# Performance work log

Measured on AMD Instinct MI355X. Metric: run time of the kernel, lower is better.

Reference implementation:

```python
import jax, jax.numpy as jnp
import numpy as np

L, B, D, Di, N, H, P, K, M, V = 4, 8, 2048, 4096, 128, 64, 64, 4, 8, 50288
Cch = Di + 2 * N           # conv channels = 4352
Dout = 2 * Di + 2 * N + H  # in_proj out = 8512
EPS = 1e-5


def _rms(x, w):
    return x * jax.lax.rsqrt(jnp.mean(x * x, axis=-1, keepdims=True) + EPS) * w


def setup_inputs() -> dict:
    key = jax.random.key(0)
    ks = jax.random.split(key, 16)
    s = 0.02
    return {
        "input_ids": jax.random.randint(ks[0], (B, 1), 0, V),
        "emb": jax.random.normal(ks[1], (V, D)) * s,
        "in_proj_w": jax.random.normal(ks[2], (L, D, Dout)) * s,
        "conv_w": jax.random.normal(ks[3], (L, Cch, K)) * s,
        "conv_b": jax.random.normal(ks[4], (L, Cch)) * s,
        "A_log": jax.random.normal(ks[5], (L, H)) * 0.5,
        "dt_bias": jax.random.normal(ks[6], (L, H)) * 0.5,
        "D_param": jax.random.normal(ks[7], (L, H)) * 0.5,
        "mixer_norm_w": jnp.ones((L, Di)),
        "out_proj_w": jax.random.normal(ks[8], (L, Di, D)) * s,
        "layer_norm_w": jnp.ones((L, D)),
        "norm_f_w": jnp.ones((D,)),
        "W_mc": jax.random.normal(ks[9], (L, M + 1)).at[:, -1].set(5.0),
        "conv_state": jax.random.normal(ks[10], (L, B, Cch, K)) * 0.1,
        "ssm_state": jax.random.normal(ks[11], (L, B, H, P, N)) * 0.1,
        "cached_states": jax.random.normal(ks[12], (L, B, M, H, P, N)) * 0.1,
    }


def reference(input_ids, emb, in_proj_w, conv_w, conv_b, A_log, dt_bias, D_param,
              mixer_norm_w, out_proj_w, layer_norm_w, norm_f_w, W_mc,
              conv_state, ssm_state, cached_states):
    ids = input_ids[:, 0]              # (B,)
    res = emb[ids]                     # (B, D) token embedding gather
    for l in range(L):
        xn = _rms(res, layer_norm_w[l])
        zxbcdt = xn @ in_proj_w[l]     # (B, Dout)
        z = zxbcdt[:, :Di]
        xBC = zxbcdt[:, Di:Di + Cch]
        dt = zxbcdt[:, Di + Cch:]
        # circular conv-state shift + depthwise conv over kernel dim
        cs = jnp.concatenate([conv_state[l][:, :, 1:], xBC[:, :, None]], axis=-1)
        xBC = jax.nn.silu(jnp.sum(cs * conv_w[l][None], axis=-1) + conv_b[l])
        x, Bm, Cm = xBC[:, :Di], xBC[:, Di:Di + N], xBC[:, Di + N:]
        dt = jax.nn.softplus(dt + dt_bias[l])                 # (B, H)
        dA = jnp.exp(dt * (-jnp.exp(A_log[l])))               # (B, H)
        x = x.reshape(B, H, P)
        dBx = jnp.einsum('bh,bn,bhp->bhpn', dt, Bm, x)        # (B,H,P,N)
        ssm = ssm_state[l] * dA[:, :, None, None] + dBx       # (B,H,P,N)
        # softmax-weighted fusion of cached segment states + current state
        w = jax.nn.softmax(W_mc[l])                           # (M+1,)
        fused = jnp.einsum('bmhpn,m->bhpn', cached_states[l], w[:-1]) + w[-1] * ssm
        y = jnp.einsum('bhpn,bn->bhp', fused, Cm) + D_param[l][None, :, None] * x
        y = y.reshape(B, Di)
        y = _rms(y * jax.nn.silu(z), mixer_norm_w[l])         # gated RMSNorm
        res = res + y @ out_proj_w[l]
    res = _rms(res, norm_f_w)
    logits = res @ emb.T               # tied lm_head
    return logits[:, None, :]          # (B, 1, V)
```

## Files before the change

kernel.cpp:

```cpp
#include <hip/hip_runtime.h>
#include <hip/hip_bf16.h>
#include <math.h>

#define LN 4
#define B_ 8
#define D_ 2048
#define DI 4096
#define N_ 128
#define H_ 64
#define P_ 64
#define K_ 4
#define M_ 8
#define V_ 50288
#define CCH (DI + 2*N_)
#define DOUT (2*DI + 2*N_ + H_)
#define EPSF 1e-5f
#define KT_IN 32
#define KT_OUT 128

typedef float f32x4 __attribute__((ext_vector_type(4)));

__device__ inline float wave_sum(float v) {
  #pragma unroll
  for (int off = 32; off > 0; off >>= 1) v += __shfl_xor(v, off, 64);
  return v;
}

__device__ inline float fold_reduce8(const float a[8], int lane) {
  float t0[4];
  #pragma unroll
  for (int r = 0; r < 4; ++r) {
    float keep = (lane & 1) ? a[2*r+1] : a[2*r];
    float send = (lane & 1) ? a[2*r]   : a[2*r+1];
    t0[r] = keep + __shfl_xor(send, 1, 64);
  }
  float t1[2];
  #pragma unroll
  for (int r = 0; r < 2; ++r) {
    float keep = (lane & 2) ? t0[2*r+1] : t0[2*r];
    float send = (lane & 2) ? t0[2*r]   : t0[2*r+1];
    t1[r] = keep + __shfl_xor(send, 2, 64);
  }
  float keep = (lane & 4) ? t1[1] : t1[0];
  float send = (lane & 4) ? t1[0] : t1[1];
  float u = keep + __shfl_xor(send, 4, 64);
  u += __shfl_xor(u, 8, 64);
  u += __shfl_xor(u, 16, 64);
  u += __shfl_xor(u, 32, 64);
  return u;
}

__global__ __launch_bounds__(256)
void k_rmsnorm(const float* __restrict__ in, const float* __restrict__ w,
               float* __restrict__ out, const int* __restrict__ ids,
               const float* __restrict__ emb, float* __restrict__ res_out) {
  __shared__ float lds[4];
  int b = blockIdx.x, tid = threadIdx.x;
  const float* row = ids ? (emb + (size_t)ids[b] * D_) : (in + (size_t)b * D_);
  f32x4 v0 = *reinterpret_cast<const f32x4*>(row + tid * 8);
  f32x4 v1 = *reinterpret_cast<const f32x4*>(row + tid * 8 + 4);
  if (res_out) {
    *reinterpret_cast<f32x4*>(res_out + (size_t)b * D_ + tid * 8)     = v0;
    *reinterpret_cast<f32x4*>(res_out + (size_t)b * D_ + tid * 8 + 4) = v1;
  }
  float ss = v0[0]*v0[0] + v0[1]*v0[1] + v0[2]*v0[2] + v0[3]*v0[3]
           + v1[0]*v1[0] + v1[1]*v1[1] + v1[2]*v1[2] + v1[3]*v1[3];
  float wsum = wave_sum(ss);
  int lane = tid & 63, wid = tid >> 6;
  if (lane == 0) lds[wid] = wsum;
  __syncthreads();
  float tot = lds[0] + lds[1] + lds[2] + lds[3];
  float scale = rsqrtf(tot / (float)D_ + EPSF);
  f32x4 w0 = *reinterpret_cast<const f32x4*>(w + tid * 8);
  f32x4 w1 = *reinterpret_cast<const f32x4*>(w + tid * 8 + 4);
  f32x4 o0 = v0 * scale * w0, o1 = v1 * scale * w1;
  *reinterpret_cast<f32x4*>(out + (size_t)b * D_ + tid * 8)     = o0;
  *reinterpret_cast<f32x4*>(out + (size_t)b * D_ + tid * 8 + 4) = o1;
}

__global__ void k_inproj1(const float* __restrict__ xn, const float* __restrict__ W,
                          float* __restrict__ pin) {
  __shared__ float xs[8][64];
  int jt = blockIdx.x % 9, kt = blockIdx.x / 9;
  int k0 = kt * 64;
  for (int i = threadIdx.x; i < 8 * 64; i += 256) {
    int r = i >> 6, kk = i & 63;
    xs[r][kk] = xn[r * D_ + k0 + kk];
  }
  __syncthreads();
  int j = jt * 1024 + threadIdx.x * 4;
  if (j >= DOUT) return;
  f32x4 acc[8];
  #pragma unroll
  for (int r = 0; r < 8; ++r) acc[r] = (f32x4)0.f;
  const float* Wp = W + (size_t)k0 * DOUT + j;
  for (int kk = 0; kk < 64; ++kk) {
    f32x4 w4 = __builtin_nontemporal_load(
        reinterpret_cast<const f32x4*>(Wp + (size_t)kk * DOUT));
    #pragma unroll
    for (int r = 0; r < 8; ++r) acc[r] += w4 * xs[r][kk];
  }
  #pragma unroll
  for (int r = 0; r < 8; ++r)
    *reinterpret_cast<f32x4*>(&pin[((size_t)kt * 8 + r) * DOUT + j]) = acc[r];
}

__global__ __launch_bounds__(256)
void k_inproj2_conv(const float* __restrict__ pin, const float* __restrict__ conv_state,
                    const float* __restrict__ conv_w, const float* __restrict__ conv_b,
                    const float* __restrict__ A_log, const float* __restrict__ dt_bias,
                    const float* __restrict__ W_mc,
                    float* __restrict__ zx, float* __restrict__ xbc,
                    float* __restrict__ dts, float* __restrict__ dav,
                    float* __restrict__ wmc) {
  const int TOT4 = B_ * DOUT / 4;
  int t = blockIdx.x * 256 + threadIdx.x;
  if (t >= TOT4) return;
  f32x4 s = (f32x4)0.f;
  const f32x4* p4 = reinterpret_cast<const f32x4*>(pin) + t;
  #pragma unroll 8
  for (int kt = 0; kt < KT_IN; ++kt) s += p4[(size_t)kt * TOT4];
  reinterpret_cast<f32x4*>(zx)[t] = s;
  int c4 = t * 4;
  int b = c4 / DOUT;
  int c = c4 - b * DOUT;
  #pragma unroll
  for (int e = 0; e < 4; ++e) {
    int ce = c + e;
    if (ce >= DI && ce < DI + CCH) {
      int cc = ce - DI;
      f32x4 cs4 = *reinterpret_cast<const f32x4*>(conv_state + ((size_t)b * CCH + cc) * K_);
      f32x4 cw4 = *reinterpret_cast<const f32x4*>(conv_w + (size_t)cc * K_);
      float v = cs4[1] * cw4[0] + cs4[2] * cw4[1] + cs4[3] * cw4[2]
              + s[e] * cw4[3] + conv_b[cc];
      xbc[b * CCH + cc] = v / (1.f + expf(-v));
    } else if (ce >= DI + CCH) {
      int h = ce - DI - CCH;
      float x = s[e] + dt_bias[h];
      float sp = (x > 20.f) ? x : log1pf(expf(x));
      dts[b * 64 + h] = sp;
      dav[b * 64 + h] = expf(-expf(A_log[h]) * sp);
    }
  }
  if (t == 0) {
    float mx = -1e30f;
    for (int i = 0; i < M_ + 1; ++i) mx = fmaxf(mx, W_mc[i]);
    float e2[M_ + 1], sum = 0.f;
    for (int i = 0; i < M_ + 1; ++i) { e2[i] = expf(W_mc[i] - mx); sum += e2[i]; }
    for (int i = 0; i < M_ + 1; ++i) wmc[i] = e2[i] / sum;
  }
}

__global__ __launch_bounds__(256)
void k_state(const float* __restrict__ xbc, const float* __restrict__ dts,
             const float* __restrict__ dav, const float* __restrict__ Dp_,
             const float* __restrict__ wmc, const float* __restrict__ ssm,
             const float* __restrict__ cached, float* __restrict__ y) {
  int wg = blockIdx.x * 4 + (threadIdx.x >> 6);
  int lane = threadIdx.x & 63;
  int b = wg >> 11;
  int h = (wg >> 5) & 63;
  int pp = wg & 31;
  int hf = lane >> 5, il = lane & 31;
  int p = pp * 2 + hf;
  float xv  = xbc[b * CCH + h * 64 + p];
  float dtv = dts[b * 64 + h];
  float da  = dav[b * 64 + h];
  float w8  = wmc[8];
  const f32x4* xb4 = reinterpret_cast<const f32x4*>(xbc);
  f32x4 B4 = xb4[b * (CCH / 4) + DI / 4 + il];
  f32x4 C4 = xb4[b * (CCH / 4) + DI / 4 + N_ / 4 + il];
  const f32x4* sp4 = reinterpret_cast<const f32x4*>(ssm) +
                     ((size_t)((b * H_ + h) * P_ + p)) * (N_ / 4) + il;
  const f32x4* cp4 = reinterpret_cast<const f32x4*>(cached) +
                     ((size_t)(((b * M_) * H_ + h) * P_ + p)) * (N_ / 4) + il;
  f32x4 s4 = __builtin_nontemporal_load(sp4);
  f32x4 f4 = (s4 * da + B4 * (dtv * xv)) * w8;
  #pragma unroll
  for (int m = 0; m < 8; ++m) {
    f32x4 c4 = __builtin_nontemporal_load(cp4 + (size_t)m * (H_ * P_ * N_ / 4));
    f4 += c4 * wmc[m];
  }
  f4 *= C4;
  float acc = f4[0] + f4[1] + f4[2] + f4[3];
  #pragma unroll
  for (int off = 1; off < 32; off <<= 1) acc += __shfl_xor(acc, off, 64);
  if (il == 0) y[b * DI + h * 64 + p] = acc + Dp_[h] * xv;
}

__global__ void k_gatednorm(const float* __restrict__ y, const float* __restrict__ zx,
                            const float* __restrict__ mnw, float* __restrict__ yg) {
  __shared__ float lds[8];
  int b = blockIdx.x;
  float tv[16];
  float ss = 0.f;
  #pragma unroll
  for (int t = 0; t < 16; ++t) {
    int i = threadIdx.x + t * 256;
    float z = zx[b * DOUT + i];
    float v = y[b * DI + i] * (z / (1.f + expf(-z)));
    tv[t] = v; ss += v * v;
  }
  float wsum = wave_sum(ss);
  int lane = threadIdx.x & 63, wid = threadIdx.x >> 6;
  if (lane == 0) lds[wid] = wsum;
  __syncthreads();
  float tot = lds[0] + lds[1] + lds[2] + lds[3];
  float scale = rsqrtf(tot / (float)DI + EPSF);
  #pragma unroll
  for (int t = 0; t < 16; ++t) {
    int i = threadIdx.x + t * 256;
    yg[b * DI + i] = tv[t] * scale * mnw[i];
  }
}

__global__ void k_outproj1(const float* __restrict__ yg, const float* __restrict__ W,
                           float* __restrict__ pout) {
  __shared__ float xs[8][32];
  int jt = blockIdx.x & 1, kt = blockIdx.x >> 1;
  int k0 = kt * 32;
  for (int i = threadIdx.x; i < 8 * 32; i += 256) {
    int r = i >> 5, kk = i & 31;
    xs[r][kk] = yg[r * DI + k0 + kk];
  }
  __syncthreads();
  int j = jt * 1024 + threadIdx.x * 4;
  f32x4 acc[8];
  #pragma unroll
  for (int r = 0; r < 8; ++r) acc[r] = (f32x4)0.f;
  const float* Wp = W + (size_t)k0 * D_ + j;
  for (int kk = 0; kk < 32; ++kk) {
    f32x4 w4 = __builtin_nontemporal_load(
        reinterpret_cast<const f32x4*>(Wp + (size_t)kk * D_));
    #pragma unroll
    for (int r = 0; r < 8; ++r) acc[r] += w4 * xs[r][kk];
  }
  #pragma unroll
  for (int r = 0; r < 8; ++r)
    *reinterpret_cast<f32x4*>(&pout[((size_t)kt * 8 + r) * D_ + j]) = acc[r];
}

__global__ __launch_bounds__(256)
void k_outproj2(const float* __restrict__ pout, float* __restrict__ res,
                float* __restrict__ zbuf, int zn4) {
  if (zbuf) {
    f32x4* z4 = reinterpret_cast<f32x4*>(zbuf);
    for (int i = blockIdx.x * 256 + threadIdx.x; i < zn4; i += 16 * 256)
      z4[i] = (f32x4)0.f;
  }
  const int TOT4 = B_ * D_ / 4;
  int t = blockIdx.x * 256 + threadIdx.x;
  f32x4 s = (f32x4)0.f;
  const f32x4* p4 = reinterpret_cast<const f32x4*>(pout) + t;
  #pragma unroll 8
  for (int kt = 0; kt < KT_OUT; ++kt) s += p4[(size_t)kt * TOT4];
  reinterpret_cast<f32x4*>(res)[t] += s;
}

#define SL_ 4
#define KS_ (D_ / SL_)
#define NVB16 (V_ / 16)
__global__ __launch_bounds__(256)
void k_logits(const float* __restrict__ xn, const float* __restrict__ emb,
              float* __restrict__ out) {
  __shared__ f32x4 xs[8][KS_ / 4];
  int s = blockIdx.x & 3, vb = blockIdx.x >> 2;
  const f32x4* xn4 = reinterpret_cast<const f32x4*>(xn);
  for (int i = threadIdx.x; i < 8 * (KS_ / 4); i += 256) {
    int r = i >> 7, q = i & 127;
    xs[r][q] = xn4[r * (D_ / 4) + s * (KS_ / 4) + q];
  }
  __syncthreads();
  int wid = threadIdx.x >> 6, lane = threadIdx.x & 63;
  int v0 = vb * 16 + wid * 4;
  const f32x4* e4 = reinterpret_cast<const f32x4*>(emb);
  #pragma unroll
  for (int vv = 0; vv < 4; ++vv) {
    int v = v0 + vv;
    const f32x4* ep = e4 + (size_t)v * (D_ / 4) + s * (KS_ / 4);
    float acc[8] = {0,0,0,0,0,0,0,0};
    #pragma unroll
    for (int st = 0; st < KS_ / 256; ++st) {
      int c = st * 64 + lane;
      f32x4 e = __builtin_nontemporal_load(ep + c);
      #pragma unroll
      for (int r = 0; r < 8; ++r) {
        f32x4 x = xs[r][c];
        acc[r] += e[0]*x[0] + e[1]*x[1] + e[2]*x[2] + e[3]*x[3];
      }
    }
    float u = fold_reduce8(acc, lane);
    if (lane < 8) atomicAdd(&out[(size_t)lane * V_ + v], u);
  }
}

extern "C" void kernel_launch(void* const* d_in, const int* in_sizes, int n_in,
                              void* d_out, int out_size, void* d_ws, size_t ws_size,
                              hipStream_t stream) {
  const int*   ids    = (const int*)  d_in[0];
  const float* emb    = (const float*)d_in[1];
  const float* inW    = (const float*)d_in[2];
  const float* convW  = (const float*)d_in[3];
  const float* convB  = (const float*)d_in[4];
  const float* Alog   = (const float*)d_in[5];
  const float* dtB    = (const float*)d_in[6];
  const float* Dpar   = (const float*)d_in[7];
  const float* mnw    = (const float*)d_in[8];
  const float* outW   = (const float*)d_in[9];
  const float* lnw    = (const float*)d_in[10];
  const float* nfw    = (const float*)d_in[11];
  const float* Wmc    = (const float*)d_in[12];
  const float* convS  = (const float*)d_in[13];
  const float* ssmS   = (const float*)d_in[14];
  const float* cached = (const float*)d_in[15];
  float* out = (float*)d_out;
  float* ws  = (float*)d_ws;

  float* res  = ws;
  float* xn   = ws + 16384;
  float* zx   = ws + 32768;
  float* xbc  = ws + 100864;
  float* dts  = ws + 135680;
  float* dav  = ws + 136192;
  float* wmc  = ws + 136704;
  float* y    = ws + 136768;
  float* yg   = ws + 169536;
  float* pin  = ws + 202304;
  float* pout = ws + 2381376;

  for (int l = 0; l < LN; ++l) {
    if (l == 0)
      k_rmsnorm<<<8, 256, 0, stream>>>(nullptr, lnw, xn, ids, emb, res);
    else
      k_rmsnorm<<<8, 256, 0, stream>>>(res, lnw + (size_t)l * D_, xn,
                                       nullptr, nullptr, nullptr);
    k_inproj1<<<288, 256, 0, stream>>>(xn, inW + (size_t)l * D_ * DOUT, pin);
    k_inproj2_conv<<<67, 256, 0, stream>>>(pin,
        convS + (size_t)l * B_ * CCH * K_, convW + (size_t)l * CCH * K_,
        convB + (size_t)l * CCH, Alog + l * H_, dtB + l * H_, Wmc + l * (M_ + 1),
        zx, xbc, dts, dav, wmc);
    k_state<<<4096, 256, 0, stream>>>(xbc, dts, dav, Dpar + l * H_, wmc,
        ssmS + (size_t)l * B_ * H_ * P_ * N_,
        cached + (size_t)l * B_ * M_ * H_ * P_ * N_, y);
    k_gatednorm<<<8, 256, 0, stream>>>(y, zx, mnw + (size_t)l * DI, yg);
    k_outproj1<<<256, 256, 0, stream>>>(yg, outW + (size_t)l * DI * D_, pout);
    k_outproj2<<<16, 256, 0, stream>>>(pout, res,
                                       (l == LN - 1) ? out : nullptr,
                                       B_ * V_ / 4);
  }
  k_rmsnorm<<<8, 256, 0, stream>>>(res, nfw, xn, nullptr, nullptr, nullptr);
  k_logits<<<NVB16 * SL_, 256, 0, stream>>>(xn, emb, out);
}
```

Measured before the change: 477.7 us.

## Fuse RMSNorm into in-proj, widen out-proj reduction, replace logit atomics with two-pass sum

The per-layer RMSNorm launch is removed. Each in-proj block now recomputes the row norms for all 8 rows and normalises its own 64-column slice. The out-proj reduction grows from 16 to 64 blocks with an in-block split-K tree, and the embedding gather for layer 0 is folded into the residual update. Logit atomics plus the output zero-fill are replaced by partial-sum stores and a separate reduction kernel. This trades fewer launches and no atomics for redundant full-row norm reads in all 288 in-proj blocks and extra partial logit traffic.

```diff
diff --git a/kernel.cpp b/kernel.cpp
--- a/kernel.cpp
+++ b/kernel.cpp
@@ -52,17 +52,12 @@
 
 __global__ __launch_bounds__(256)
 void k_rmsnorm(const float* __restrict__ in, const float* __restrict__ w,
-               float* __restrict__ out, const int* __restrict__ ids,
-               const float* __restrict__ emb, float* __restrict__ res_out) {
+               float* __restrict__ out) {
   __shared__ float lds[4];
   int b = blockIdx.x, tid = threadIdx.x;
-  const float* row = ids ? (emb + (size_t)ids[b] * D_) : (in + (size_t)b * D_);
+  const float* row = in + (size_t)b * D_;
   f32x4 v0 = *reinterpret_cast<const f32x4*>(row + tid * 8);
   f32x4 v1 = *reinterpret_cast<const f32x4*>(row + tid * 8 + 4);
-  if (res_out) {
-    *reinterpret_cast<f32x4*>(res_out + (size_t)b * D_ + tid * 8)     = v0;
-    *reinterpret_cast<f32x4*>(res_out + (size_t)b * D_ + tid * 8 + 4) = v1;
-  }
   float ss = v0[0]*v0[0] + v0[1]*v0[1] + v0[2]*v0[2] + v0[3]*v0[3]
            + v1[0]*v1[0] + v1[1]*v1[1] + v1[2]*v1[2] + v1[3]*v1[3];
   float wsum = wave_sum(ss);
@@ -78,17 +73,39 @@
   *reinterpret_cast<f32x4*>(out + (size_t)b * D_ + tid * 8 + 4) = o1;
 }
 
-__global__ void k_inproj1(const float* __restrict__ xn, const float* __restrict__ W,
-                          float* __restrict__ pin) {
+__global__ __launch_bounds__(256)
+void k_inproj1(const float* __restrict__ res, const int* __restrict__ ids,
+               const float* __restrict__ emb, const float* __restrict__ lnw,
+               const float* __restrict__ W, float* __restrict__ pin) {
   __shared__ float xs[8][64];
+  __shared__ float sred[4][8];
+  int tid = threadIdx.x, lane = tid & 63, wid = tid >> 6;
   int jt = blockIdx.x % 9, kt = blockIdx.x / 9;
   int k0 = kt * 64;
-  for (int i = threadIdx.x; i < 8 * 64; i += 256) {
+  float ssq[8];
+  #pragma unroll
+  for (int r = 0; r < 8; ++r) {
+    const float* row = ids ? (emb + (size_t)ids[r] * D_) : (res + (size_t)r * D_);
+    f32x4 a = *reinterpret_cast<const f32x4*>(row + tid * 8);
+    f32x4 c = *reinterpret_cast<const f32x4*>(row + tid * 8 + 4);
+    ssq[r] = a[0]*a[0] + a[1]*a[1] + a[2]*a[2] + a[3]*a[3]
+           + c[0]*c[0] + c[1]*c[1] + c[2]*c[2] + c[3]*c[3];
+  }
+  #pragma unroll
+  for (int r = 0; r < 8; ++r) {
+    float wsum = wave_sum(ssq[r]);
+    if (lane == 0) sred[wid][r] = wsum;
+  }
+  __syncthreads();
+  for (int i = tid; i < 8 * 64; i += 256) {
     int r = i >> 6, kk = i & 63;
-    xs[r][kk] = xn[r * D_ + k0 + kk];
-  }
-  __syncthreads();
-  int j = jt * 1024 + threadIdx.x * 4;
+    const float* row = ids ? (emb + (size_t)ids[r] * D_) : (res + (size_t)r * D_);
+    float tot = sred[0][r] + sred[1][r] + sred[2][r] + sred[3][r];
+    float scale = rsqrtf(tot / (float)D_ + EPSF);
+    xs[r][kk] = row[k0 + kk] * scale * lnw[k0 + kk];
+  }
+  __syncthreads();
+  int j = jt * 1024 + tid * 4;
   if (j >= DOUT) return;
   f32x4 acc[8];
   #pragma unroll
@@ -242,19 +259,30 @@
 
 __global__ __launch_bounds__(256)
 void k_outproj2(const float* __restrict__ pout, float* __restrict__ res,
-                float* __restrict__ zbuf, int zn4) {
-  if (zbuf) {
-    f32x4* z4 = reinterpret_cast<f32x4*>(zbuf);
-    for (int i = blockIdx.x * 256 + threadIdx.x; i < zn4; i += 16 * 256)
-      z4[i] = (f32x4)0.f;
-  }
+                const int* __restrict__ ids, const float* __restrict__ emb) {
+  __shared__ f32x4 red[256];
   const int TOT4 = B_ * D_ / 4;
-  int t = blockIdx.x * 256 + threadIdx.x;
+  int tid = threadIdx.x;
+  int pos = blockIdx.x * 64 + (tid & 63);
+  int kq = tid >> 6;
+  const f32x4* p4 = reinterpret_cast<const f32x4*>(pout) + pos;
   f32x4 s = (f32x4)0.f;
-  const f32x4* p4 = reinterpret_cast<const f32x4*>(pout) + t;
   #pragma unroll 8
-  for (int kt = 0; kt < KT_OUT; ++kt) s += p4[(size_t)kt * TOT4];
-  reinterpret_cast<f32x4*>(res)[t] += s;
+  for (int k = 0; k < 32; ++k)
+    s += p4[(size_t)(kq * 32 + k) * TOT4];
+  red[tid] = s;
+  __syncthreads();
+  if (tid < 64) {
+    f32x4 tot = red[tid] + red[tid + 64] + red[tid + 128] + red[tid + 192];
+    f32x4* r4 = reinterpret_cast<f32x4*>(res);
+    if (ids) {
+      int b = pos >> 9, d4 = pos & 511;
+      f32x4 base = reinterpret_cast<const f32x4*>(emb)[(size_t)ids[b] * (D_ / 4) + d4];
+      r4[pos] = base + tot;
+    } else {
+      r4[pos] += tot;
+    }
+  }
 }
 
 #define SL_ 4
@@ -262,7 +290,7 @@
 #define NVB16 (V_ / 16)
 __global__ __launch_bounds__(256)
 void k_logits(const float* __restrict__ xn, const float* __restrict__ emb,
-              float* __restrict__ out) {
+              float* __restrict__ pl) {
   __shared__ f32x4 xs[8][KS_ / 4];
   int s = blockIdx.x & 3, vb = blockIdx.x >> 2;
   const f32x4* xn4 = reinterpret_cast<const f32x4*>(xn);
@@ -290,8 +318,20 @@
       }
     }
     float u = fold_reduce8(acc, lane);
-    if (lane < 8) atomicAdd(&out[(size_t)lane * V_ + v], u);
-  }
+    if (lane < 8) pl[((size_t)s * 8 + lane) * V_ + v] = u;
+  }
+}
+
+__global__ __launch_bounds__(256)
+void k_logits2(const float* __restrict__ pl, float* __restrict__ out) {
+  int v = blockIdx.x * 256 + threadIdx.x;
+  if (v >= V_) return;
+  int r = blockIdx.y;
+  float t = pl[(size_t)r * V_ + v]
+          + pl[((size_t)8  + r) * V_ + v]
+          + pl[((size_t)16 + r) * V_ + v]
+          + pl[((size_t)24 + r) * V_ + v];
+  out[(size_t)r * V_ + v] = t;
 }
 
 extern "C" void kernel_launch(void* const* d_in, const int* in_sizes, int n_in,
@@ -327,14 +367,12 @@
   float* yg   = ws + 169536;
   float* pin  = ws + 202304;
   float* pout = ws + 2381376;
+  float* pl   = ws + 4478528;
 
   for (int l = 0; l < LN; ++l) {
-    if (l == 0)
-      k_rmsnorm<<<8, 256, 0, stream>>>(nullptr, lnw, xn, ids, emb, res);
-    else
-      k_rmsnorm<<<8, 256, 0, stream>>>(res, lnw + (size_t)l * D_, xn,
-                                       nullptr, nullptr, nullptr);
-    k_inproj1<<<288, 256, 0, stream>>>(xn, inW + (size_t)l * D_ * DOUT, pin);
+    k_inproj1<<<288, 256, 0, stream>>>(res, (l == 0) ? ids : nullptr, emb,
+                                       lnw + (size_t)l * D_,
+                                       inW + (size_t)l * D_ * DOUT, pin);
     k_inproj2_conv<<<67, 256, 0, stream>>>(pin,
         convS + (size_t)l * B_ * CCH * K_, convW + (size_t)l * CCH * K_,
         convB + (size_t)l * CCH, Alog + l * H_, dtB + l * H_, Wmc + l * (M_ + 1),
@@ -344,10 +382,10 @@
         cached + (size_t)l * B_ * M_ * H_ * P_ * N_, y);
     k_gatednorm<<<8, 256, 0, stream>>>(y, zx, mnw + (size_t)l * DI, yg);
     k_outproj1<<<256, 256, 0, stream>>>(yg, outW + (size_t)l * DI * D_, pout);
-    k_outproj2<<<16, 256, 0, stream>>>(pout, res,
-                                       (l == LN - 1) ? out : nullptr,
-                                       B_ * V_ / 4);
-  }
-  k_rmsnorm<<<8, 256, 0, stream>>>(res, nfw, xn, nullptr, nullptr, nullptr);
-  k_logits<<<NVB16 * SL_, 256, 0, stream>>>(xn, emb, out);
-}
+    k_outproj2<<<64, 256, 0, stream>>>(pout, res,
+                                       (l == 0) ? ids : nullptr, emb);
+  }
+  k_rmsnorm<<<8, 256, 0, stream>>>(res, nfw, xn);
+  k_logits<<<NVB16 * SL_, 256, 0, stream>>>(xn, emb, pl);
+  k_logits2<<<dim3((V_ + 255) / 256, 8), 256, 0, stream>>>(pl, out);
+}
```

Result: faster. 435.5 us (-8.8%).
